# Optimization experiments

Measured on AMD Instinct MI355X. Metric: run time of the kernel, lower is better.

The kernel has to match this reference:

```python
import jax, jax.numpy as jnp
import numpy as np

B, T, D, H, L = 128, 512, 512, 512, 256


def setup_inputs() -> dict:
    key = jax.random.key(0)
    ks = jax.random.split(key, 7)
    lim = 1.0 / np.sqrt(H)
    u = lambda k, shape, lo: jax.random.uniform(k, shape, jnp.float32, -lo, lo)
    x = jax.random.normal(ks[0], (B, T, D), dtype=jnp.float32)
    Wih = u(ks[1], (3 * H, D), lim)
    Whh = u(ks[2], (3 * H, H), lim)
    b = u(ks[3], (3 * H,), lim)
    bn = u(ks[4], (H,), lim)
    lim_l = 1.0 / np.sqrt(H)
    Wlin = u(ks[5], (2 * L, H), lim_l)
    blin = u(ks[6], (2 * L,), lim_l)
    return {"x": x, "Wih": Wih, "Whh": Whh, "b": b, "bn": bn, "Wlin": Wlin, "blin": blin}


def reference(x, Wih, Whh, b, bn, Wlin, blin):
    # x: (B, T, D). Batched GRU recurrence over time via lax.scan.
    def step(h, xt):
        ig = xt @ Wih.T + b           # (B, 3H)
        hg = h @ Whh.T                # (B, 3H)
        ir, iz, inn = jnp.split(ig, 3, axis=-1)
        hr, hz, hn = jnp.split(hg, 3, axis=-1)
        r = jax.nn.sigmoid(ir + hr)
        z = jax.nn.sigmoid(iz + hz)
        n = jnp.tanh(inn + r * (hn + bn))
        h_new = (1.0 - z) * n + z * h
        return h_new, None

    xs = jnp.swapaxes(x, 0, 1)        # (T, B, D)
    h0 = jnp.zeros((x.shape[0], Whh.shape[1]), dtype=x.dtype)
    h_final, _ = jax.lax.scan(step, h0, xs)
    out = h_final @ Wlin.T + blin     # (B, 2L)
    mu, logvar = jnp.split(out, 2, axis=-1)
    return (mu, logvar)
```

## Files before the change

### kernel.cpp

```cpp
#include <hip/hip_runtime.h>
#include <stdint.h>


typedef short short8 __attribute__((ext_vector_type(8)));
typedef float f32x4 __attribute__((ext_vector_type(4)));
typedef int int4v __attribute__((ext_vector_type(4)));

#define NB 128
#define NT 512
#define ND 512
#define NH 512
#define NG 1536

__device__ __forceinline__ unsigned short f2bf(float f) {
  union { float f; unsigned u; } v; v.f = f;
  unsigned r = v.u + 0x7fffu + ((v.u >> 16) & 1u);
  return (unsigned short)(r >> 16);
}
__device__ __forceinline__ float bf2f(unsigned short u) {
  union { unsigned u; float f; } v; v.u = ((unsigned)u) << 16; return v.f;
}
__device__ __forceinline__ float sigmoid_f(float x) {
  float e = __builtin_amdgcn_exp2f(-1.4426950408889634f * x);
  return __builtin_amdgcn_rcpf(1.0f + e);
}
__device__ __forceinline__ float tanh_f(float x) {
  float e = __builtin_amdgcn_exp2f(2.8853900817779268f * x);
  return 1.0f - 2.0f * __builtin_amdgcn_rcpf(1.0f + e);
}
__device__ __forceinline__ short8 pack8(float4 a, float4 b) {
  short8 s;
  s[0] = (short)f2bf(a.x); s[1] = (short)f2bf(a.y);
  s[2] = (short)f2bf(a.z); s[3] = (short)f2bf(a.w);
  s[4] = (short)f2bf(b.x); s[5] = (short)f2bf(b.y);
  s[6] = (short)f2bf(b.z); s[7] = (short)f2bf(b.w);
  return s;
}

__device__ __forceinline__ void load_h16(const unsigned short* p, int4v a[16]) {
  asm volatile(
      "global_load_dwordx4 %0,  %16, off sc1\n\t"
      "global_load_dwordx4 %1,  %16, off offset:64 sc1\n\t"
      "global_load_dwordx4 %2,  %16, off offset:128 sc1\n\t"
      "global_load_dwordx4 %3,  %16, off offset:192 sc1\n\t"
      "global_load_dwordx4 %4,  %16, off offset:256 sc1\n\t"
      "global_load_dwordx4 %5,  %16, off offset:320 sc1\n\t"
      "global_load_dwordx4 %6,  %16, off offset:384 sc1\n\t"
      "global_load_dwordx4 %7,  %16, off offset:448 sc1\n\t"
      "global_load_dwordx4 %8,  %16, off offset:512 sc1\n\t"
      "global_load_dwordx4 %9,  %16, off offset:576 sc1\n\t"
      "global_load_dwordx4 %10, %16, off offset:640 sc1\n\t"
      "global_load_dwordx4 %11, %16, off offset:704 sc1\n\t"
      "global_load_dwordx4 %12, %16, off offset:768 sc1\n\t"
      "global_load_dwordx4 %13, %16, off offset:832 sc1\n\t"
      "global_load_dwordx4 %14, %16, off offset:896 sc1\n\t"
      "global_load_dwordx4 %15, %16, off offset:960 sc1\n\t"
      "s_waitcnt vmcnt(0)"
      : "=&v"(a[0]), "=&v"(a[1]), "=&v"(a[2]), "=&v"(a[3]),
        "=&v"(a[4]), "=&v"(a[5]), "=&v"(a[6]), "=&v"(a[7]),
        "=&v"(a[8]), "=&v"(a[9]), "=&v"(a[10]), "=&v"(a[11]),
        "=&v"(a[12]), "=&v"(a[13]), "=&v"(a[14]), "=&v"(a[15])
      : "v"(p)
      : "memory");
}

__device__ __forceinline__ void store_h4(unsigned short* p, unsigned v0,
                                         unsigned v1, unsigned v2, unsigned v3) {
  asm volatile(
      "global_store_short %0, %1, off sc1\n\t"
      "global_store_short %0, %2, off offset:1024 sc1\n\t"
      "global_store_short %0, %3, off offset:2048 sc1\n\t"
      "global_store_short %0, %4, off offset:3072 sc1\n\t"
      "s_waitcnt vmcnt(0)"
      :
      : "v"(p), "v"(v0), "v"(v1), "v"(v2), "v"(v3)
      : "memory");
}

__device__ __forceinline__ unsigned poll_load_dev(const unsigned* p) {
  unsigned f;
  asm volatile(
      "global_load_dword %0, %1, off sc1\n\t"
      "s_waitcnt vmcnt(0)"
      : "=v"(f) : "v"(p) : "memory");
  return f;
}

__device__ __forceinline__ unsigned poll_load_sys(const unsigned* p) {
  unsigned f;
  asm volatile(
      "global_load_dword %0, %1, off sc0 sc1\n\t"
      "s_waitcnt vmcnt(0)"
      : "=v"(f) : "v"(p) : "memory");
  return f;
}

__device__ __forceinline__ void flag_store(unsigned* p, unsigned v) {
  asm volatile("global_store_dword %0, %1, off sc1"
               :: "v"(p), "v"(v) : "memory");
}

__global__ __launch_bounds__(256) void ig_gemm(
    const float* __restrict__ x, const float* __restrict__ Wih,
    const float* __restrict__ bias, unsigned short* __restrict__ IG) {
  __shared__ unsigned short As[128 * 40];
  __shared__ unsigned short Bs[128 * 40];
  const int tid = threadIdx.x;
  const int bm = blockIdx.x, bn = blockIdx.y;
  const int lane = tid & 63, w = tid >> 6;
  const int wm = w >> 1, wn = w & 1;
  const int l15 = lane & 15, q = lane >> 4;

  f32x4 acc[4][4] = {};

  for (int kt = 0; kt < 16; ++kt) {
    __syncthreads();
#pragma unroll
    for (int j = 0; j < 4; ++j) {
      int fi = tid + 256 * j;
      int row = fi >> 3, kq = fi & 7;
      float4 v = *(const float4*)(x + (size_t)(bm * 128 + row) * ND + kt * 32 + kq * 4);
      ushort4 s = {f2bf(v.x), f2bf(v.y), f2bf(v.z), f2bf(v.w)};
      *(ushort4*)&As[row * 40 + kq * 4] = s;
    }
#pragma unroll
    for (int j = 0; j < 4; ++j) {
      int fi = tid + 256 * j;
      int row = fi >> 3, kq = fi & 7;
      float4 v = *(const float4*)(Wih + (size_t)(bn * 128 + row) * ND + kt * 32 + kq * 4);
      ushort4 s = {f2bf(v.x), f2bf(v.y), f2bf(v.z), f2bf(v.w)};
      *(ushort4*)&Bs[row * 40 + kq * 4] = s;
    }
    __syncthreads();

    short8 af[4], bfv[4];
#pragma unroll
    for (int tm = 0; tm < 4; ++tm)
      af[tm] = *(const short8*)&As[(wm * 64 + tm * 16 + l15) * 40 + q * 8];
#pragma unroll
    for (int tn = 0; tn < 4; ++tn)
      bfv[tn] = *(const short8*)&Bs[(wn * 64 + tn * 16 + l15) * 40 + q * 8];
#pragma unroll
    for (int tm = 0; tm < 4; ++tm)
#pragma unroll
      for (int tn = 0; tn < 4; ++tn)
        acc[tm][tn] = __builtin_amdgcn_mfma_f32_16x16x32_bf16(af[tm], bfv[tn], acc[tm][tn], 0, 0, 0);
  }

#pragma unroll
  for (int tm = 0; tm < 4; ++tm) {
#pragma unroll
    for (int tn = 0; tn < 4; ++tn) {
      int col = bn * 128 + wn * 64 + tn * 16 + l15;
      float bb = bias[col];
#pragma unroll
      for (int i = 0; i < 4; ++i) {
        int row = bm * 128 + wm * 64 + tm * 16 + q * 4 + i;
        IG[(size_t)row * NG + col] = f2bf(acc[tm][tn][i] + bb);
      }
    }
  }
}

template <bool USE_IG>
__global__ __launch_bounds__(256, 1) void gru_rec(
    const float* __restrict__ x, const float* __restrict__ Wih,
    const float* __restrict__ Whh, const float* __restrict__ bias,
    const float* __restrict__ bn, const unsigned short* __restrict__ IG,
    unsigned short* __restrict__ hbuf, unsigned* __restrict__ flags,
    float* __restrict__ hfin) {
  const int tid = threadIdx.x;
  const int lane = tid & 63;
  const int w = tid >> 6;
  const int wm = w >> 1, wn = w & 1;
  const int l15 = lane & 15, q = lane >> 4;
  const int g = blockIdx.x >> 4;
  const int c = blockIdx.x & 15;
  const int b0 = g * 32;
  const int col = c * 32 + wn * 16 + l15;
  const int mrow = b0 + wm * 16 + l15;
  const int erow = b0 + wm * 16 + q * 4;

  unsigned* const myflag = flags + ((g * 2 + wm) * 16 + c) * 2 + wn;
  const unsigned* const pollbase = flags + (g * 2 + wm) * 32;

  short8 bfr[3][16];
#pragma unroll
  for (int gt = 0; gt < 3; ++gt) {
    const float* src = Whh + (size_t)(gt * NH + col) * NH + q * 8;
#pragma unroll
    for (int kk = 0; kk < 16; ++kk) {
      float4 v0 = *(const float4*)(src + kk * 32);
      float4 v1 = *(const float4*)(src + kk * 32 + 4);
      bfr[gt][kk] = pack8(v0, v1);
    }
  }

  float bi_r = 0.f, bi_z = 0.f, bi_n = 0.f;
  if (!USE_IG) {
    bi_r = bias[col];
    bi_z = bias[NH + col];
    bi_n = bias[2 * NH + col];
  }
  const float bnv = bn[col];

  float hreg[4] = {0.f, 0.f, 0.f, 0.f};

  unsigned short* const hb0 = hbuf;
  unsigned short* const hb1 = hbuf + NB * NH;

  for (int t = 0; t < NT; ++t) {
    const unsigned short* hcur = (t & 1) ? hb1 : hb0;
    unsigned short* hnxt = (t & 1) ? hb0 : hb1;

    float igr[4], igz[4], ign[4];
    if (USE_IG) {
#pragma unroll
      for (int i = 0; i < 4; ++i) {
        const size_t base = ((size_t)(erow + i) * NT + t) * NG + col;
        igr[i] = bf2f(IG[base]);
        igz[i] = bf2f(IG[base + NH]);
        ign[i] = bf2f(IG[base + 2 * NH]);
      }
    }

    int4v araw[16];
    if (t > 0) {
      if (lane < 32) {
        const unsigned* fp = pollbase + lane;
        unsigned f = poll_load_dev(fp);
        int tries = 0;
        while ((int)f < t) {
          if (++tries > 8) f = poll_load_sys(fp);
          else             f = poll_load_dev(fp);
        }
      }
      load_h16(hcur + (size_t)mrow * NH + q * 8, araw);
    } else {
#pragma unroll
      for (int kk = 0; kk < 16; ++kk) araw[kk] = (int4v){0, 0, 0, 0};
    }

    f32x4 ar = {0.f, 0.f, 0.f, 0.f};
    f32x4 az = {0.f, 0.f, 0.f, 0.f};
    f32x4 an = {0.f, 0.f, 0.f, 0.f};
    f32x4 ai = {0.f, 0.f, 0.f, 0.f};
#pragma unroll
    for (int kk = 0; kk < 16; ++kk) {
      short8 afk = __builtin_bit_cast(short8, araw[kk]);
      ar = __builtin_amdgcn_mfma_f32_16x16x32_bf16(afk, bfr[0][kk], ar, 0, 0, 0);
      az = __builtin_amdgcn_mfma_f32_16x16x32_bf16(afk, bfr[1][kk], az, 0, 0, 0);
      an = __builtin_amdgcn_mfma_f32_16x16x32_bf16(afk, bfr[2][kk], an, 0, 0, 0);
      if (!USE_IG) {
        const float* xp = x + ((size_t)mrow * NT + t) * ND + kk * 32 + q * 8;
        short8 xa = pack8(*(const float4*)xp, *(const float4*)(xp + 4));
#pragma unroll
        for (int gt = 0; gt < 3; ++gt) {
          const float* wp = Wih + (size_t)(gt * NH + col) * ND + kk * 32 + q * 8;
          short8 wf = pack8(*(const float4*)wp, *(const float4*)(wp + 4));
          if (gt == 0) ar = __builtin_amdgcn_mfma_f32_16x16x32_bf16(xa, wf, ar, 0, 0, 0);
          if (gt == 1) az = __builtin_amdgcn_mfma_f32_16x16x32_bf16(xa, wf, az, 0, 0, 0);
          if (gt == 2) ai = __builtin_amdgcn_mfma_f32_16x16x32_bf16(xa, wf, ai, 0, 0, 0);
        }
      }
    }

    unsigned sv[4];
#pragma unroll
    for (int i = 0; i < 4; ++i) {
      float xr = USE_IG ? (ar[i] + igr[i]) : (ar[i] + bi_r);
      float xz = USE_IG ? (az[i] + igz[i]) : (az[i] + bi_z);
      float xin = USE_IG ? ign[i] : (ai[i] + bi_n);
      float r = sigmoid_f(xr);
      float z = sigmoid_f(xz);
      float n = tanh_f(xin + r * (an[i] + bnv));
      float hn2 = (1.f - z) * n + z * hreg[i];
      hreg[i] = hn2;
      sv[i] = (unsigned)f2bf(hn2);
      if (t == NT - 1) hfin[(size_t)(erow + i) * NH + col] = hn2;
    }
    if (t != NT - 1) {
      store_h4(hnxt + (size_t)erow * NH + col, sv[0], sv[1], sv[2], sv[3]);
      if (lane == 0) flag_store(myflag, (unsigned)(t + 1));
    }
  }
}

__global__ __launch_bounds__(256) void final_linear(
    const float* __restrict__ hfin, const float* __restrict__ Wlin,
    const float* __restrict__ blin, float* __restrict__ out) {
  __shared__ float sh[16 * 516];
  const int tid = threadIdx.x;
  const int b0 = blockIdx.y * 16, o0 = blockIdx.x * 16;

  for (int j = tid; j < 16 * 128; j += 256) {
    int row = j >> 7, kq = j & 127;
    *(float4*)&sh[row * 516 + kq * 4] =
        *(const float4*)(hfin + (size_t)(b0 + row) * NH + kq * 4);
  }
  __syncthreads();

  const int bi = tid & 15, oi = tid >> 4;
  const int o = o0 + oi;
  const float4* wp = (const float4*)(Wlin + (size_t)o * NH);
  float4 a4 = {0.f, 0.f, 0.f, 0.f};
  for (int k4 = 0; k4 < 128; ++k4) {
    float4 wv = wp[k4];
    float4 hv = *(const float4*)&sh[bi * 516 + k4 * 4];
    a4.x += wv.x * hv.x; a4.y += wv.y * hv.y;
    a4.z += wv.z * hv.z; a4.w += wv.w * hv.w;
  }
  float v = a4.x + a4.y + a4.z + a4.w + blin[o];
  int b = b0 + bi;
  if (o < 256) out[b * 256 + o] = v;
  else out[32768 + b * 256 + (o - 256)] = v;
}

extern "C" void kernel_launch(void* const* d_in, const int* in_sizes, int n_in,
                              void* d_out, int out_size, void* d_ws, size_t ws_size,
                              hipStream_t stream) {
  const float* x    = (const float*)d_in[0];
  const float* Wih  = (const float*)d_in[1];
  const float* Whh  = (const float*)d_in[2];
  const float* bias = (const float*)d_in[3];
  const float* bn   = (const float*)d_in[4];
  const float* Wlin = (const float*)d_in[5];
  const float* blin = (const float*)d_in[6];
  float* out = (float*)d_out;

  char* ws = (char*)d_ws;
  unsigned short* hbuf = (unsigned short*)ws;
  unsigned* flags      = (unsigned*)(ws + 262144);
  float* hfin          = (float*)(ws + 263168);
  unsigned short* IG   = (unsigned short*)(ws + 525312);
  const size_t need_min = 525312;
  const size_t need_ig  = 525312 + (size_t)NB * NT * NG * 2;
  if (ws_size < need_min) return;

  hipMemsetAsync(ws + 262144, 0, 1024, stream);

  const bool useIG = (ws_size >= need_ig);
  if (useIG) {
    ig_gemm<<<dim3(512, 12), 256, 0, stream>>>(x, Wih, bias, IG);
    gru_rec<true><<<64, 256, 0, stream>>>(x, Wih, Whh, bias, bn, IG, hbuf, flags, hfin);
  } else {
    gru_rec<false><<<64, 256, 0, stream>>>(x, Wih, Whh, bias, bn, nullptr, hbuf, flags, hfin);
  }
  final_linear<<<dim3(32, 8), 256, 0, stream>>>(hfin, Wlin, blin, out);
}
```

Baseline: 2.268 ms.

## Fuse input-gate GEMM into recurrent kernel with producer/consumer flag overlap

Merges the separate input-gate GEMM and the GRU recurrence into one persistent launch. 64 blocks run the recurrence while 192 extra blocks compute IG tiles, ordered by time quarter, and publish per-tile ready flags with coherent stores. Recurrent blocks poll those flags every 128 timesteps before reading IG. This hides the GEMM behind the serial recurrence, at the cost of relying on all 256 blocks being co-resident and adding coherent-store and polling overhead.

Measured after the change: 2.259 ms, median of 2. Within noise of the previous version (-0.4%).

```diff
diff --git a/kernel.cpp b/kernel.cpp
--- a/kernel.cpp
+++ b/kernel.cpp
@@ -99,81 +99,97 @@
   asm volatile("global_store_dword %0, %1, off sc1"
                :: "v"(p), "v"(v) : "memory");
 }
-
-__global__ __launch_bounds__(256) void ig_gemm(
+__device__ __forceinline__ void flag_store_sys(unsigned* p, unsigned v) {
+  asm volatile("global_store_dword %0, %1, off sc0 sc1"
+               :: "v"(p), "v"(v) : "memory");
+}
+__device__ __forceinline__ void store_short_coh(unsigned short* p, unsigned v) {
+  asm volatile("global_store_short %0, %1, off sc0 sc1"
+               :: "v"(p), "v"(v) : "memory");
+}
+
+template <bool USE_IG>
+__global__ __launch_bounds__(256, 1) void gru_fused(
     const float* __restrict__ x, const float* __restrict__ Wih,
-    const float* __restrict__ bias, unsigned short* __restrict__ IG) {
+    const float* __restrict__ Whh, const float* __restrict__ bias,
+    const float* __restrict__ bn, unsigned short* __restrict__ IG,
+    unsigned short* __restrict__ hbuf, unsigned* __restrict__ hflags,
+    unsigned* __restrict__ igflags, float* __restrict__ hfin) {
   __shared__ unsigned short As[128 * 40];
   __shared__ unsigned short Bs[128 * 40];
-  const int tid = threadIdx.x;
-  const int bm = blockIdx.x, bn = blockIdx.y;
-  const int lane = tid & 63, w = tid >> 6;
-  const int wm = w >> 1, wn = w & 1;
-  const int l15 = lane & 15, q = lane >> 4;
-
-  f32x4 acc[4][4] = {};
-
-  for (int kt = 0; kt < 16; ++kt) {
-    __syncthreads();
-#pragma unroll
-    for (int j = 0; j < 4; ++j) {
-      int fi = tid + 256 * j;
-      int row = fi >> 3, kq = fi & 7;
-      float4 v = *(const float4*)(x + (size_t)(bm * 128 + row) * ND + kt * 32 + kq * 4);
-      ushort4 s = {f2bf(v.x), f2bf(v.y), f2bf(v.z), f2bf(v.w)};
-      *(ushort4*)&As[row * 40 + kq * 4] = s;
-    }
-#pragma unroll
-    for (int j = 0; j < 4; ++j) {
-      int fi = tid + 256 * j;
-      int row = fi >> 3, kq = fi & 7;
-      float4 v = *(const float4*)(Wih + (size_t)(bn * 128 + row) * ND + kt * 32 + kq * 4);
-      ushort4 s = {f2bf(v.x), f2bf(v.y), f2bf(v.z), f2bf(v.w)};
-      *(ushort4*)&Bs[row * 40 + kq * 4] = s;
-    }
-    __syncthreads();
-
-    short8 af[4], bfv[4];
-#pragma unroll
-    for (int tm = 0; tm < 4; ++tm)
-      af[tm] = *(const short8*)&As[(wm * 64 + tm * 16 + l15) * 40 + q * 8];
-#pragma unroll
-    for (int tn = 0; tn < 4; ++tn)
-      bfv[tn] = *(const short8*)&Bs[(wn * 64 + tn * 16 + l15) * 40 + q * 8];
-#pragma unroll
-    for (int tm = 0; tm < 4; ++tm)
-#pragma unroll
-      for (int tn = 0; tn < 4; ++tn)
-        acc[tm][tn] = __builtin_amdgcn_mfma_f32_16x16x32_bf16(af[tm], bfv[tn], acc[tm][tn], 0, 0, 0);
-  }
-
-#pragma unroll
-  for (int tm = 0; tm < 4; ++tm) {
-#pragma unroll
-    for (int tn = 0; tn < 4; ++tn) {
-      int col = bn * 128 + wn * 64 + tn * 16 + l15;
-      float bb = bias[col];
-#pragma unroll
-      for (int i = 0; i < 4; ++i) {
-        int row = bm * 128 + wm * 64 + tm * 16 + q * 4 + i;
-        IG[(size_t)row * NG + col] = f2bf(acc[tm][tn][i] + bb);
-      }
-    }
-  }
-}
-
-template <bool USE_IG>
-__global__ __launch_bounds__(256, 1) void gru_rec(
-    const float* __restrict__ x, const float* __restrict__ Wih,
-    const float* __restrict__ Whh, const float* __restrict__ bias,
-    const float* __restrict__ bn, const unsigned short* __restrict__ IG,
-    unsigned short* __restrict__ hbuf, unsigned* __restrict__ flags,
-    float* __restrict__ hfin) {
+
   const int tid = threadIdx.x;
   const int lane = tid & 63;
   const int w = tid >> 6;
   const int wm = w >> 1, wn = w & 1;
   const int l15 = lane & 15, q = lane >> 4;
+
+  if (USE_IG && blockIdx.x >= 64) {
+    const int pid = blockIdx.x - 64;
+    for (int T = pid; T < 6144; T += 192) {
+      const int qt = T / 1536;
+      const int rem = T - qt * 1536;
+      const int b = rem / 12;
+      const int bnn = rem - b * 12;
+      const int bm = b * 4 + qt;
+
+      f32x4 acc[4][4] = {};
+      for (int kt = 0; kt < 16; ++kt) {
+        __syncthreads();
+#pragma unroll
+        for (int j = 0; j < 4; ++j) {
+          int fi = tid + 256 * j;
+          int row = fi >> 3, kq = fi & 7;
+          float4 v = *(const float4*)(x + (size_t)(bm * 128 + row) * ND + kt * 32 + kq * 4);
+          ushort4 s = {f2bf(v.x), f2bf(v.y), f2bf(v.z), f2bf(v.w)};
+          *(ushort4*)&As[row * 40 + kq * 4] = s;
+        }
+#pragma unroll
+        for (int j = 0; j < 4; ++j) {
+          int fi = tid + 256 * j;
+          int row = fi >> 3, kq = fi & 7;
+          float4 v = *(const float4*)(Wih + (size_t)(bnn * 128 + row) * ND + kt * 32 + kq * 4);
+          ushort4 s = {f2bf(v.x), f2bf(v.y), f2bf(v.z), f2bf(v.w)};
+          *(ushort4*)&Bs[row * 40 + kq * 4] = s;
+        }
+        __syncthreads();
+
+        short8 af[4], bfv[4];
+#pragma unroll
+        for (int tm = 0; tm < 4; ++tm)
+          af[tm] = *(const short8*)&As[(wm * 64 + tm * 16 + l15) * 40 + q * 8];
+#pragma unroll
+        for (int tn = 0; tn < 4; ++tn)
+          bfv[tn] = *(const short8*)&Bs[(wn * 64 + tn * 16 + l15) * 40 + q * 8];
+#pragma unroll
+        for (int tm = 0; tm < 4; ++tm)
+#pragma unroll
+          for (int tn = 0; tn < 4; ++tn)
+            acc[tm][tn] = __builtin_amdgcn_mfma_f32_16x16x32_bf16(af[tm], bfv[tn], acc[tm][tn], 0, 0, 0);
+      }
+
+#pragma unroll
+      for (int tm = 0; tm < 4; ++tm) {
+#pragma unroll
+        for (int tn = 0; tn < 4; ++tn) {
+          int ccol = bnn * 128 + wn * 64 + tn * 16 + l15;
+          float bb = bias[ccol];
+#pragma unroll
+          for (int i = 0; i < 4; ++i) {
+            int row = bm * 128 + wm * 64 + tm * 16 + q * 4 + i;
+            store_short_coh(IG + (size_t)row * NG + ccol,
+                            (unsigned)f2bf(acc[tm][tn][i] + bb));
+          }
+        }
+      }
+      asm volatile("s_waitcnt vmcnt(0)" ::: "memory");
+      __syncthreads();
+      if (tid == 0) flag_store_sys(igflags + bm * 12 + bnn, 1u);
+    }
+    return;
+  }
+  if (!USE_IG && blockIdx.x >= 64) return;
+
   const int g = blockIdx.x >> 4;
   const int c = blockIdx.x & 15;
   const int b0 = g * 32;
@@ -181,8 +197,8 @@
   const int mrow = b0 + wm * 16 + l15;
   const int erow = b0 + wm * 16 + q * 4;
 
-  unsigned* const myflag = flags + ((g * 2 + wm) * 16 + c) * 2 + wn;
-  const unsigned* const pollbase = flags + (g * 2 + wm) * 32;
+  unsigned* const myflag = hflags + ((g * 2 + wm) * 16 + c) * 2 + wn;
+  const unsigned* const pollbase = hflags + (g * 2 + wm) * 32;
 
   short8 bfr[3][16];
 #pragma unroll
@@ -212,6 +228,19 @@
   for (int t = 0; t < NT; ++t) {
     const unsigned short* hcur = (t & 1) ? hb1 : hb0;
     unsigned short* hnxt = (t & 1) ? hb0 : hb1;
+
+    if (USE_IG && (t & 127) == 0) {
+      const int qt = t >> 7;
+      if (lane < 32) {
+        const int bb = b0 + lane;
+#pragma unroll
+        for (int gi = 0; gi < 3; ++gi) {
+          const unsigned* fp = igflags + (size_t)(bb * 4 + qt) * 12 + (c >> 2) + gi * 4;
+          unsigned f = poll_load_sys(fp);
+          while (f == 0u) f = poll_load_sys(fp);
+        }
+      }
+    }
 
     float igr[4], igz[4], ign[4];
     if (USE_IG) {
@@ -330,21 +359,23 @@
 
   char* ws = (char*)d_ws;
   unsigned short* hbuf = (unsigned short*)ws;
-  unsigned* flags      = (unsigned*)(ws + 262144);
-  float* hfin          = (float*)(ws + 263168);
-  unsigned short* IG   = (unsigned short*)(ws + 525312);
-  const size_t need_min = 525312;
-  const size_t need_ig  = 525312 + (size_t)NB * NT * NG * 2;
+  unsigned* hflags     = (unsigned*)(ws + 262144);
+  unsigned* igflags    = (unsigned*)(ws + 263168);
+  float* hfin          = (float*)(ws + 287744);
+  unsigned short* IG   = (unsigned short*)(ws + 549888);
+  const size_t need_min = 549888;
+  const size_t need_ig  = 549888 + (size_t)NB * NT * NG * 2;
   if (ws_size < need_min) return;
 
-  hipMemsetAsync(ws + 262144, 0, 1024, stream);
+  hipMemsetAsync(ws + 262144, 0, 1024 + 24576, stream);
 
   const bool useIG = (ws_size >= need_ig);
   if (useIG) {
-    ig_gemm<<<dim3(512, 12), 256, 0, stream>>>(x, Wih, bias, IG);
-    gru_rec<true><<<64, 256, 0, stream>>>(x, Wih, Whh, bias, bn, IG, hbuf, flags, hfin);
+    gru_fused<true><<<256, 256, 0, stream>>>(x, Wih, Whh, bias, bn, IG,
+                                             hbuf, hflags, igflags, hfin);
   } else {
-    gru_rec<false><<<64, 256, 0, stream>>>(x, Wih, Whh, bias, bn, nullptr, hbuf, flags, hfin);
+    gru_fused<false><<<64, 256, 0, stream>>>(x, Wih, Whh, bias, bn, nullptr,
+                                             hbuf, hflags, igflags, hfin);
   }
   final_linear<<<dim3(32, 8), 256, 0, stream>>>(hfin, Wlin, blin, out);
 }
```

## Fuse input projection into recurrent kernel with Wih slice cached in LDS

Applied to the files above, without the earlier changes.

Removes the separate ig_gemm pre-pass and its large bf16 IG buffer, and instead computes the x·Wih projection inside each recurrent step. Each block stages its bf16 Wih column slice (96 KB) in shared memory once. The input-projection MFMAs are issued before polling for the previous hidden state, so they can overlap the inter-block wait. The trade-off is more per-step work on the serial critical path: 64 blocks must read x from fp32 and convert it every step.

After: 4.665 ms. 2.06x slower.

```diff
diff --git a/kernel.cpp b/kernel.cpp
--- a/kernel.cpp
+++ b/kernel.cpp
@@ -10,15 +10,11 @@
 #define NT 512
 #define ND 512
 #define NH 512
-#define NG 1536
 
 __device__ __forceinline__ unsigned short f2bf(float f) {
   union { float f; unsigned u; } v; v.f = f;
   unsigned r = v.u + 0x7fffu + ((v.u >> 16) & 1u);
   return (unsigned short)(r >> 16);
-}
-__device__ __forceinline__ float bf2f(unsigned short u) {
-  union { unsigned u; float f; } v; v.u = ((unsigned)u) << 16; return v.f;
 }
 __device__ __forceinline__ float sigmoid_f(float x) {
   float e = __builtin_amdgcn_exp2f(-1.4426950408889634f * x);
@@ -85,7 +81,6 @@
       : "=v"(f) : "v"(p) : "memory");
   return f;
 }
-
 __device__ __forceinline__ unsigned poll_load_sys(const unsigned* p) {
   unsigned f;
   asm volatile(
@@ -94,81 +89,18 @@
       : "=v"(f) : "v"(p) : "memory");
   return f;
 }
-
 __device__ __forceinline__ void flag_store(unsigned* p, unsigned v) {
   asm volatile("global_store_dword %0, %1, off sc1"
                :: "v"(p), "v"(v) : "memory");
 }
 
-__global__ __launch_bounds__(256) void ig_gemm(
-    const float* __restrict__ x, const float* __restrict__ Wih,
-    const float* __restrict__ bias, unsigned short* __restrict__ IG) {
-  __shared__ unsigned short As[128 * 40];
-  __shared__ unsigned short Bs[128 * 40];
-  const int tid = threadIdx.x;
-  const int bm = blockIdx.x, bn = blockIdx.y;
-  const int lane = tid & 63, w = tid >> 6;
-  const int wm = w >> 1, wn = w & 1;
-  const int l15 = lane & 15, q = lane >> 4;
-
-  f32x4 acc[4][4] = {};
-
-  for (int kt = 0; kt < 16; ++kt) {
-    __syncthreads();
-#pragma unroll
-    for (int j = 0; j < 4; ++j) {
-      int fi = tid + 256 * j;
-      int row = fi >> 3, kq = fi & 7;
-      float4 v = *(const float4*)(x + (size_t)(bm * 128 + row) * ND + kt * 32 + kq * 4);
-      ushort4 s = {f2bf(v.x), f2bf(v.y), f2bf(v.z), f2bf(v.w)};
-      *(ushort4*)&As[row * 40 + kq * 4] = s;
-    }
-#pragma unroll
-    for (int j = 0; j < 4; ++j) {
-      int fi = tid + 256 * j;
-      int row = fi >> 3, kq = fi & 7;
-      float4 v = *(const float4*)(Wih + (size_t)(bn * 128 + row) * ND + kt * 32 + kq * 4);
-      ushort4 s = {f2bf(v.x), f2bf(v.y), f2bf(v.z), f2bf(v.w)};
-      *(ushort4*)&Bs[row * 40 + kq * 4] = s;
-    }
-    __syncthreads();
-
-    short8 af[4], bfv[4];
-#pragma unroll
-    for (int tm = 0; tm < 4; ++tm)
-      af[tm] = *(const short8*)&As[(wm * 64 + tm * 16 + l15) * 40 + q * 8];
-#pragma unroll
-    for (int tn = 0; tn < 4; ++tn)
-      bfv[tn] = *(const short8*)&Bs[(wn * 64 + tn * 16 + l15) * 40 + q * 8];
-#pragma unroll
-    for (int tm = 0; tm < 4; ++tm)
-#pragma unroll
-      for (int tn = 0; tn < 4; ++tn)
-        acc[tm][tn] = __builtin_amdgcn_mfma_f32_16x16x32_bf16(af[tm], bfv[tn], acc[tm][tn], 0, 0, 0);
-  }
-
-#pragma unroll
-  for (int tm = 0; tm < 4; ++tm) {
-#pragma unroll
-    for (int tn = 0; tn < 4; ++tn) {
-      int col = bn * 128 + wn * 64 + tn * 16 + l15;
-      float bb = bias[col];
-#pragma unroll
-      for (int i = 0; i < 4; ++i) {
-        int row = bm * 128 + wm * 64 + tm * 16 + q * 4 + i;
-        IG[(size_t)row * NG + col] = f2bf(acc[tm][tn][i] + bb);
-      }
-    }
-  }
-}
-
-template <bool USE_IG>
 __global__ __launch_bounds__(256, 1) void gru_rec(
     const float* __restrict__ x, const float* __restrict__ Wih,
     const float* __restrict__ Whh, const float* __restrict__ bias,
-    const float* __restrict__ bn, const unsigned short* __restrict__ IG,
-    unsigned short* __restrict__ hbuf, unsigned* __restrict__ flags,
-    float* __restrict__ hfin) {
+    const float* __restrict__ bn, unsigned short* __restrict__ hbuf,
+    unsigned* __restrict__ flags, float* __restrict__ hfin) {
+  __shared__ short8 Wlds[3 * 16 * 4 * 32];
+
   const int tid = threadIdx.x;
   const int lane = tid & 63;
   const int w = tid >> 6;
@@ -180,9 +112,23 @@
   const int col = c * 32 + wn * 16 + l15;
   const int mrow = b0 + wm * 16 + l15;
   const int erow = b0 + wm * 16 + q * 4;
+  const int ci = wn * 16 + l15;
 
   unsigned* const myflag = flags + ((g * 2 + wm) * 16 + c) * 2 + wn;
   const unsigned* const pollbase = flags + (g * 2 + wm) * 32;
+
+#pragma unroll
+  for (int j = 0; j < 24; ++j) {
+    int fid = tid + 256 * j;
+    int gate = fid >> 11;
+    int rem = fid & 2047;
+    int kk = rem >> 7;
+    int q2 = (rem >> 5) & 3;
+    int colIdx = rem & 31;
+    const float* src = Wih + (size_t)(gate * NH + c * 32 + colIdx) * ND + kk * 32 + q2 * 8;
+    Wlds[((gate * 16 + kk) * 4 + q2) * 32 + colIdx] =
+        pack8(*(const float4*)src, *(const float4*)(src + 4));
+  }
 
   short8 bfr[3][16];
 #pragma unroll
@@ -195,13 +141,11 @@
       bfr[gt][kk] = pack8(v0, v1);
     }
   }
-
-  float bi_r = 0.f, bi_z = 0.f, bi_n = 0.f;
-  if (!USE_IG) {
-    bi_r = bias[col];
-    bi_z = bias[NH + col];
-    bi_n = bias[2 * NH + col];
-  }
+  __syncthreads();
+
+  const float bi_r = bias[col];
+  const float bi_z = bias[NH + col];
+  const float bi_n = bias[2 * NH + col];
   const float bnv = bn[col];
 
   float hreg[4] = {0.f, 0.f, 0.f, 0.f};
@@ -213,15 +157,20 @@
     const unsigned short* hcur = (t & 1) ? hb1 : hb0;
     unsigned short* hnxt = (t & 1) ? hb0 : hb1;
 
-    float igr[4], igz[4], ign[4];
-    if (USE_IG) {
-#pragma unroll
-      for (int i = 0; i < 4; ++i) {
-        const size_t base = ((size_t)(erow + i) * NT + t) * NG + col;
-        igr[i] = bf2f(IG[base]);
-        igz[i] = bf2f(IG[base + NH]);
-        ign[i] = bf2f(IG[base + 2 * NH]);
-      }
+    f32x4 ar = {0.f, 0.f, 0.f, 0.f};
+    f32x4 az = {0.f, 0.f, 0.f, 0.f};
+    f32x4 an = {0.f, 0.f, 0.f, 0.f};
+    f32x4 ai = {0.f, 0.f, 0.f, 0.f};
+#pragma unroll
+    for (int kk = 0; kk < 16; ++kk) {
+      const float* xp = x + ((size_t)mrow * NT + t) * ND + kk * 32 + q * 8;
+      short8 xa = pack8(*(const float4*)xp, *(const float4*)(xp + 4));
+      const short8 wr = Wlds[((0 * 16 + kk) * 4 + q) * 32 + ci];
+      const short8 wz = Wlds[((1 * 16 + kk) * 4 + q) * 32 + ci];
+      const short8 wn8 = Wlds[((2 * 16 + kk) * 4 + q) * 32 + ci];
+      ar = __builtin_amdgcn_mfma_f32_16x16x32_bf16(xa, wr, ar, 0, 0, 0);
+      az = __builtin_amdgcn_mfma_f32_16x16x32_bf16(xa, wz, az, 0, 0, 0);
+      ai = __builtin_amdgcn_mfma_f32_16x16x32_bf16(xa, wn8, ai, 0, 0, 0);
     }
 
     int4v araw[16];
@@ -236,41 +185,21 @@
         }
       }
       load_h16(hcur + (size_t)mrow * NH + q * 8, araw);
-    } else {
-#pragma unroll
-      for (int kk = 0; kk < 16; ++kk) araw[kk] = (int4v){0, 0, 0, 0};
-    }
-
-    f32x4 ar = {0.f, 0.f, 0.f, 0.f};
-    f32x4 az = {0.f, 0.f, 0.f, 0.f};
-    f32x4 an = {0.f, 0.f, 0.f, 0.f};
-    f32x4 ai = {0.f, 0.f, 0.f, 0.f};
-#pragma unroll
-    for (int kk = 0; kk < 16; ++kk) {
-      short8 afk = __builtin_bit_cast(short8, araw[kk]);
-      ar = __builtin_amdgcn_mfma_f32_16x16x32_bf16(afk, bfr[0][kk], ar, 0, 0, 0);
-      az = __builtin_amdgcn_mfma_f32_16x16x32_bf16(afk, bfr[1][kk], az, 0, 0, 0);
-      an = __builtin_amdgcn_mfma_f32_16x16x32_bf16(afk, bfr[2][kk], an, 0, 0, 0);
-      if (!USE_IG) {
-        const float* xp = x + ((size_t)mrow * NT + t) * ND + kk * 32 + q * 8;
-        short8 xa = pack8(*(const float4*)xp, *(const float4*)(xp + 4));
-#pragma unroll
-        for (int gt = 0; gt < 3; ++gt) {
-          const float* wp = Wih + (size_t)(gt * NH + col) * ND + kk * 32 + q * 8;
-          short8 wf = pack8(*(const float4*)wp, *(const float4*)(wp + 4));
-          if (gt == 0) ar = __builtin_amdgcn_mfma_f32_16x16x32_bf16(xa, wf, ar, 0, 0, 0);
-          if (gt == 1) az = __builtin_amdgcn_mfma_f32_16x16x32_bf16(xa, wf, az, 0, 0, 0);
-          if (gt == 2) ai = __builtin_amdgcn_mfma_f32_16x16x32_bf16(xa, wf, ai, 0, 0, 0);
-        }
+#pragma unroll
+      for (int kk = 0; kk < 16; ++kk) {
+        short8 afk = __builtin_bit_cast(short8, araw[kk]);
+        ar = __builtin_amdgcn_mfma_f32_16x16x32_bf16(afk, bfr[0][kk], ar, 0, 0, 0);
+        az = __builtin_amdgcn_mfma_f32_16x16x32_bf16(afk, bfr[1][kk], az, 0, 0, 0);
+        an = __builtin_amdgcn_mfma_f32_16x16x32_bf16(afk, bfr[2][kk], an, 0, 0, 0);
       }
     }
 
     unsigned sv[4];
 #pragma unroll
     for (int i = 0; i < 4; ++i) {
-      float xr = USE_IG ? (ar[i] + igr[i]) : (ar[i] + bi_r);
-      float xz = USE_IG ? (az[i] + igz[i]) : (az[i] + bi_z);
-      float xin = USE_IG ? ign[i] : (ai[i] + bi_n);
+      float xr = ar[i] + bi_r;
+      float xz = az[i] + bi_z;
+      float xin = ai[i] + bi_n;
       float r = sigmoid_f(xr);
       float z = sigmoid_f(xz);
       float n = tanh_f(xin + r * (an[i] + bnv));
@@ -332,19 +261,11 @@
   unsigned short* hbuf = (unsigned short*)ws;
   unsigned* flags      = (unsigned*)(ws + 262144);
   float* hfin          = (float*)(ws + 263168);
-  unsigned short* IG   = (unsigned short*)(ws + 525312);
   const size_t need_min = 525312;
-  const size_t need_ig  = 525312 + (size_t)NB * NT * NG * 2;
   if (ws_size < need_min) return;
 
   hipMemsetAsync(ws + 262144, 0, 1024, stream);
 
-  const bool useIG = (ws_size >= need_ig);
-  if (useIG) {
-    ig_gemm<<<dim3(512, 12), 256, 0, stream>>>(x, Wih, bias, IG);
-    gru_rec<true><<<64, 256, 0, stream>>>(x, Wih, Whh, bias, bn, IG, hbuf, flags, hfin);
-  } else {
-    gru_rec<false><<<64, 256, 0, stream>>>(x, Wih, Whh, bias, bn, nullptr, hbuf, flags, hfin);
-  }
+  gru_rec<<<64, 256, 0, stream>>>(x, Wih, Whh, bias, bn, hbuf, flags, hfin);
   final_linear<<<dim3(32, 8), 256, 0, stream>>>(hfin, Wlin, blin, out);
 }
```
